# Kernel tuning notes

Measured on AMD Instinct MI355X. Metric: run time of the kernel, lower is better.

The kernel has to match this reference:

```python
import jax, jax.numpy as jnp
import numpy as np

# dims: T=tgt_len, B=batch, A=n_agents, S=src_len, V=vocab, N_OOV=out-of-vocab slots
T, B, A, S, V, N_OOV = 64, 8, 3, 400, 50000, 400
V_EXT = V + N_OOV


def setup_inputs() -> dict:
    key = jax.random.key(0)
    k1, k2, k3, k4, k5 = jax.random.split(key, 5)
    article = jax.random.randint(k1, (S, B, A), 0, V_EXT)
    vocab_probs = jax.nn.softmax(jax.random.normal(k2, (T, B, V), dtype=jnp.float32), axis=-1)
    generation_probs = jax.nn.sigmoid(jax.random.normal(k3, (T, B, A), dtype=jnp.float32))
    agentwise_attn = jax.nn.softmax(jax.random.normal(k4, (T, B, A, S), dtype=jnp.float32), axis=-1)
    agent_attn = jax.nn.softmax(jax.random.normal(k5, (T, B, A), dtype=jnp.float32), axis=-1)
    return {"article": article, "vocab_probs": vocab_probs,
            "generation_probs": generation_probs, "agentwise_attn": agentwise_attn,
            "agent_attn": agent_attn}


def reference(article, vocab_probs, generation_probs, agentwise_attn, agent_attn):
    # pointer-generator mix, per (t, b, agent)
    gen = generation_probs[..., None]                      # [T,B,A,1]
    voc_gen = gen * vocab_probs[:, :, None, :]             # [T,B,A,V]
    copy_w = (1.0 - gen) * agentwise_attn                  # [T,B,A,S]
    # scatter_add copy weights into extended vocab at article token ids
    idx = jnp.transpose(article, (1, 2, 0))                # [B,A,S]
    idx = jnp.broadcast_to(idx[None], (T, B, A, S)).reshape(T * B * A, S)
    ext = jnp.zeros((T * B * A, V_EXT), vocab_probs.dtype)
    ext = ext.at[jnp.arange(T * B * A)[:, None], idx].add(copy_w.reshape(T * B * A, S))
    ext = ext.reshape(T, B, A, V_EXT)
    ext = ext.at[..., :V].add(voc_gen)                     # generation part on base vocab
    # weighted sum over agents -> [T,B,V_EXT]
    return jnp.einsum('tba,tbav->tbv', agent_attn, ext)
```

## Files before the change

kernel.cpp:

```cpp
#include <hip/hip_runtime.h>

constexpr int T = 64, B = 8, A = 3, S = 400, V = 50000, N_OOV = 400;
constexpr int V_EXT  = V + N_OOV;
constexpr int NSUB   = 4;
constexpr int C_SUB  = V_EXT / NSUB;
constexpr int C4_SUB = C_SUB / 4;
constexpr int V4     = V / 4;
constexpr int NTHR   = 512;
constexpr int FULL_K = C4_SUB / NTHR;

__global__ __launch_bounds__(NTHR) void pg_lds_kernel(
    const int*   __restrict__ article,
    const float* __restrict__ vocab_probs,
    const float* __restrict__ gen_probs,
    const float* __restrict__ agentwise_attn,
    const float* __restrict__ agent_attn,
    float*       __restrict__ out)
{
    __shared__ float acc[C_SUB];
    const int bid = blockIdx.x;
    const int tb  = bid >> 2;
    const int sub = bid & 3;
    const int b   = tb % B;
    const int tid = threadIdx.x;

    float4* acc4 = reinterpret_cast<float4*>(acc);
    for (int j = tid; j < C4_SUB; j += NTHR)
        acc4[j] = make_float4(0.f, 0.f, 0.f, 0.f);

    float coef = 0.f;
    float cw[A];
#pragma unroll
    for (int a = 0; a < A; ++a) {
        const float aa = agent_attn[tb * A + a];
        const float g  = gen_probs[tb * A + a];
        coef += aa * g;
        cw[a] = aa * (1.f - g);
    }

    __syncthreads();

    const int lo = sub * C_SUB;
    const int hi = lo + C_SUB;
    const float* aw = agentwise_attn + (size_t)tb * A * S;
    for (int i2 = tid; i2 < A * S; i2 += NTHR) {
        const int a   = (i2 >= 2 * S) ? 2 : (i2 >= S ? 1 : 0);
        const int s   = i2 - a * S;
        const int idx = article[(s * B + b) * A + a];
        if (idx >= lo && idx < hi)
            atomicAdd(&acc[idx - lo], cw[a] * aw[i2]);
    }

    __syncthreads();

    const float4* vp4  = reinterpret_cast<const float4*>(vocab_probs + (size_t)tb * V);
    float4*       out4 = reinterpret_cast<float4*>(out + (size_t)tb * V_EXT);
    const int base = sub * C4_SUB;
    const int i0   = base + tid;

    float4 v[FULL_K];
#pragma unroll
    for (int k = 0; k < FULL_K; ++k) {
        const int i  = i0 + k * NTHR;
        const int ic = (i < V4) ? i : (V4 - 1);
        v[k] = vp4[ic];
    }
#pragma unroll
    for (int k = 0; k < FULL_K; ++k) {
        const int i = i0 + k * NTHR;
        float4 r = acc4[i - base];
        if (i < V4) {
            r.x += coef * v[k].x;  r.y += coef * v[k].y;
            r.z += coef * v[k].z;  r.w += coef * v[k].w;
        }
        out4[i] = r;
    }
    const int it = i0 + FULL_K * NTHR;
    if (it < base + C4_SUB) {
        float4 r = acc4[it - base];
        if (it < V4) {
            const float4 vv = vp4[it];
            r.x += coef * vv.x;  r.y += coef * vv.y;
            r.z += coef * vv.z;  r.w += coef * vv.w;
        }
        out4[it] = r;
    }
}

extern "C" void kernel_launch(void* const* d_in, const int* in_sizes, int n_in,
                              void* d_out, int out_size, void* d_ws, size_t ws_size,
                              hipStream_t stream) {
    const int*   article        = (const int*)  d_in[0];
    const float* vocab_probs    = (const float*)d_in[1];
    const float* gen_probs      = (const float*)d_in[2];
    const float* agentwise_attn = (const float*)d_in[3];
    const float* agent_attn     = (const float*)d_in[4];
    float*       out            = (float*)d_out;

    pg_lds_kernel<<<dim3(T * B * NSUB), dim3(NTHR), 0, stream>>>(
        article, vocab_probs, gen_probs, agentwise_attn, agent_attn, out);
}
```

Measured before the change: 39.68 us.

## Prefetch scatter inputs and vocab tiles before LDS accumulation, split into six slices

The article indices, attention values and all vocab_probs float4 loads (including the tail) are now issued into registers before the LDS zero-fill and atomic scatter. This lets global memory latency overlap with the shared-memory work instead of serialising the phases. The vocab range per (t,b) is split into 6 slices instead of 4, which gives more, smaller blocks and less LDS per block, and launch bounds ask for 8 blocks per CU. The cost is more registers per thread and each block reading the full 1200 scatter inputs for a smaller slice.

Result: faster. 37.86 us (-4.6%).

```diff
diff --git a/kernel.cpp b/kernel.cpp
--- a/kernel.cpp
+++ b/kernel.cpp
@@ -2,14 +2,15 @@
 
 constexpr int T = 64, B = 8, A = 3, S = 400, V = 50000, N_OOV = 400;
 constexpr int V_EXT  = V + N_OOV;
-constexpr int NSUB   = 4;
+constexpr int NSUB   = 6;
 constexpr int C_SUB  = V_EXT / NSUB;
 constexpr int C4_SUB = C_SUB / 4;
 constexpr int V4     = V / 4;
 constexpr int NTHR   = 512;
 constexpr int FULL_K = C4_SUB / NTHR;
+constexpr int NSC    = 3;
 
-__global__ __launch_bounds__(NTHR) void pg_lds_kernel(
+__global__ __launch_bounds__(NTHR, 8) void pg_pipe_kernel(
     const int*   __restrict__ article,
     const float* __restrict__ vocab_probs,
     const float* __restrict__ gen_probs,
@@ -19,14 +20,10 @@
 {
     __shared__ float acc[C_SUB];
     const int bid = blockIdx.x;
-    const int tb  = bid >> 2;
-    const int sub = bid & 3;
+    const int tb  = bid / NSUB;
+    const int sub = bid - tb * NSUB;
     const int b   = tb % B;
     const int tid = threadIdx.x;
-
-    float4* acc4 = reinterpret_cast<float4*>(acc);
-    for (int j = tid; j < C4_SUB; j += NTHR)
-        acc4[j] = make_float4(0.f, 0.f, 0.f, 0.f);
 
     float coef = 0.f;
     float cw[A];
@@ -38,20 +35,20 @@
         cw[a] = aa * (1.f - g);
     }
 
-    __syncthreads();
-
-    const int lo = sub * C_SUB;
-    const int hi = lo + C_SUB;
+    int   sidx[NSC];
+    float sraw[NSC];
     const float* aw = agentwise_attn + (size_t)tb * A * S;
-    for (int i2 = tid; i2 < A * S; i2 += NTHR) {
-        const int a   = (i2 >= 2 * S) ? 2 : (i2 >= S ? 1 : 0);
-        const int s   = i2 - a * S;
-        const int idx = article[(s * B + b) * A + a];
-        if (idx >= lo && idx < hi)
-            atomicAdd(&acc[idx - lo], cw[a] * aw[i2]);
+#pragma unroll
+    for (int j = 0; j < NSC; ++j) {
+        const int i2 = tid + j * NTHR;
+        sidx[j] = -1; sraw[j] = 0.f;
+        if (i2 < A * S) {
+            const int a = (i2 >= 2 * S) ? 2 : (i2 >= S ? 1 : 0);
+            const int s = i2 - a * S;
+            sidx[j] = article[(s * B + b) * A + a];
+            sraw[j] = aw[i2];
+        }
     }
-
-    __syncthreads();
 
     const float4* vp4  = reinterpret_cast<const float4*>(vocab_probs + (size_t)tb * V);
     float4*       out4 = reinterpret_cast<float4*>(out + (size_t)tb * V_EXT);
@@ -65,6 +62,28 @@
         const int ic = (i < V4) ? i : (V4 - 1);
         v[k] = vp4[ic];
     }
+    const int  it       = i0 + FULL_K * NTHR;
+    const bool has_tail = (it < base + C4_SUB);
+    float4 vt = make_float4(0.f, 0.f, 0.f, 0.f);
+    if (has_tail) vt = vp4[(it < V4) ? it : (V4 - 1)];
+
+    float4* acc4 = reinterpret_cast<float4*>(acc);
+    for (int j = tid; j < C4_SUB; j += NTHR)
+        acc4[j] = make_float4(0.f, 0.f, 0.f, 0.f);
+    __syncthreads();
+
+    const int lo = sub * C_SUB;
+    const int hi = lo + C_SUB;
+#pragma unroll
+    for (int j = 0; j < NSC; ++j) {
+        if (sidx[j] >= lo && sidx[j] < hi) {
+            const int i2 = tid + j * NTHR;
+            const int a  = (i2 >= 2 * S) ? 2 : (i2 >= S ? 1 : 0);
+            atomicAdd(&acc[sidx[j] - lo], cw[a] * sraw[j]);
+        }
+    }
+    __syncthreads();
+
 #pragma unroll
     for (int k = 0; k < FULL_K; ++k) {
         const int i = i0 + k * NTHR;
@@ -75,13 +94,11 @@
         }
         out4[i] = r;
     }
-    const int it = i0 + FULL_K * NTHR;
-    if (it < base + C4_SUB) {
+    if (has_tail) {
         float4 r = acc4[it - base];
         if (it < V4) {
-            const float4 vv = vp4[it];
-            r.x += coef * vv.x;  r.y += coef * vv.y;
-            r.z += coef * vv.z;  r.w += coef * vv.w;
+            r.x += coef * vt.x;  r.y += coef * vt.y;
+            r.z += coef * vt.z;  r.w += coef * vt.w;
         }
         out4[it] = r;
     }
@@ -97,6 +114,6 @@
     const float* agent_attn     = (const float*)d_in[4];
     float*       out            = (float*)d_out;
 
-    pg_lds_kernel<<<dim3(T * B * NSUB), dim3(NTHR), 0, stream>>>(
+    pg_pipe_kernel<<<dim3(T * B * NSUB), dim3(NTHR), 0, stream>>>(
         article, vocab_probs, gen_probs, agentwise_attn, agent_attn, out);
 }
```
